# Performance work log

Measured on AMD Instinct MI355X. Metric: run time of the kernel, lower is better.

The kernel has to match this reference:

```python
import jax, jax.numpy as jnp
import numpy as np
import math

B, LT, LS, D, H, DFF = 4, 1024, 1024, 1024, 16, 4096
DK = D // H
EPS = 1e-5


def setup_inputs() -> dict:
    key = jax.random.key(0)
    ks = jax.random.split(key, 32)
    n = lambda i, shape, s=0.02: jax.random.normal(ks[i], shape, jnp.float32) * s
    inp = {
        'tgt': jax.random.normal(ks[0], (B, LT, D), jnp.float32),
        'memory': jax.random.normal(ks[1], (B, LS, D), jnp.float32),
        'src_pad_mask': jnp.zeros((B, LT, LS), dtype=bool),
        'tgt_mask': jnp.broadcast_to(jnp.triu(jnp.ones((LT, LT), dtype=bool), 1), (B, LT, LT)),
        # self-attention projections
        'self_wq': n(2, (D, D)), 'self_bq': jnp.zeros((D,)),
        'self_wk': n(3, (D, D)), 'self_bk': jnp.zeros((D,)),
        'self_wv': n(4, (D, D)), 'self_bv': jnp.zeros((D,)),
        'self_wo': n(5, (D, D)), 'self_bo': jnp.zeros((D,)),
        # cross-attention projections
        'cross_wq': n(6, (D, D)), 'cross_bq': jnp.zeros((D,)),
        'cross_wk': n(7, (D, D)), 'cross_bk': jnp.zeros((D,)),
        'cross_wv': n(8, (D, D)), 'cross_bv': jnp.zeros((D,)),
        'cross_wo': n(9, (D, D)), 'cross_bo': jnp.zeros((D,)),
        # layer norms (pre-norm)
        'ln1_g': jnp.ones((D,)), 'ln1_b': jnp.zeros((D,)),
        'ln2_g': jnp.ones((D,)), 'ln2_b': jnp.zeros((D,)),
        'ln3_g': jnp.ones((D,)), 'ln3_b': jnp.zeros((D,)),
        # feed forward
        'ffn_w1': n(10, (D, DFF)), 'ffn_b1': jnp.zeros((DFF,)),
        'ffn_w2': n(11, (DFF, D)), 'ffn_b2': jnp.zeros((D,)),
    }
    return inp


def _layernorm(x, g, b):
    mu = jnp.mean(x, axis=-1, keepdims=True)
    var = jnp.mean(jnp.square(x - mu), axis=-1, keepdims=True)
    return (x - mu) * jax.lax.rsqrt(var + EPS) * g + b


def _mha(xq, xkv, wq, bq, wk, bk, wv, bv, wo, bo, mask):
    b, lq, d = xq.shape
    lk = xkv.shape[1]
    q = (xq @ wq + bq).reshape(b, lq, H, DK).transpose(0, 2, 1, 3) / math.sqrt(DK)
    k = (xkv @ wk + bk).reshape(b, lk, H, DK).transpose(0, 2, 1, 3)
    v = (xkv @ wv + bv).reshape(b, lk, H, DK).transpose(0, 2, 1, 3)
    scores = jnp.einsum('bhqd,bhkd->bhqk', q, k)  # [B,H,Lq,Lk]
    scores = jnp.where(mask[:, None], -1e18, scores)
    attn = jax.nn.softmax(scores, axis=-1)  # dropout p=0 (eval)
    ctx = jnp.einsum('bhqk,bhkd->bhqd', attn, v)
    ctx = ctx.transpose(0, 2, 1, 3).reshape(b, lq, d)
    return ctx @ wo + bo


def reference(tgt, memory, src_pad_mask, tgt_mask,
              self_wq, self_bq, self_wk, self_bk, self_wv, self_bv, self_wo, self_bo,
              cross_wq, cross_bq, cross_wk, cross_bk, cross_wv, cross_bv, cross_wo, cross_bo,
              ln1_g, ln1_b, ln2_g, ln2_b, ln3_g, ln3_b,
              ffn_w1, ffn_b1, ffn_w2, ffn_b2):
    # pre-norm sublayer 1: self attention
    x = tgt + _mha(_layernorm(tgt, ln1_g, ln1_b), _layernorm(tgt, ln1_g, ln1_b),
                   self_wq, self_bq, self_wk, self_bk, self_wv, self_bv, self_wo, self_bo, tgt_mask)
    # pre-norm sublayer 2: cross attention
    x = x + _mha(_layernorm(x, ln2_g, ln2_b), memory,
                 cross_wq, cross_bq, cross_wk, cross_bk, cross_wv, cross_bv, cross_wo, cross_bo, src_pad_mask)
    # pre-norm sublayer 3: FFN
    h = _layernorm(x, ln3_g, ln3_b)
    x = x + (jax.nn.gelu(h @ ffn_w1 + ffn_b1) @ ffn_w2 + ffn_b2)
    return x
```

## Files before the change

kernel.cpp:

```cpp
#include <hip/hip_runtime.h>

typedef unsigned short u16;
typedef __attribute__((ext_vector_type(8))) __bf16 bf16x8;
typedef __attribute__((ext_vector_type(4))) float floatx4;

__device__ inline float bf2f(u16 u) {
    union { unsigned int i; float f; } x; x.i = ((unsigned int)u) << 16; return x.f;
}
__device__ inline u16 f2bf(float f) {
    __bf16 h = (__bf16)f; return __builtin_bit_cast(unsigned short, h);
}
__device__ inline float load_f(u16 v) { return bf2f(v); }
__device__ inline float load_f(float v) { return v; }

__device__ inline floatx4 mfma_bf16(bf16x8 a, bf16x8 b, floatx4 c) {
    return __builtin_amdgcn_mfma_f32_16x16x32_bf16(a, b, c, 0, 0, 0);
}

__device__ inline float gelu_tanh(float x) {
    float u = 0.7978845608028654f * (x + 0.044715f * x * x * x);
    u = fminf(fmaxf(u, -15.f), 15.f);
    float e = __expf(2.f * u);
    float th = (e - 1.f) / (e + 1.f);
    return 0.5f * x * (1.f + th);
}

__device__ inline void async16(const void* g, void* l) {
    __builtin_amdgcn_global_load_lds(
        (const __attribute__((address_space(1))) unsigned int*)g,
        (__attribute__((address_space(3))) unsigned int*)l, 16, 0, 0);
}

__global__ __launch_bounds__(256)
void detect_dtype(const u16* __restrict__ p, int* __restrict__ flag) {
    int t = threadIdx.x, cnt = 0;
    #pragma unroll
    for (int j = 0; j < 8; ++j) {
        unsigned e = (p[t * 8 + j] >> 7) & 0xFF;
        cnt += (e >= 100 && e <= 140) ? 1 : 0;
    }
    __shared__ int s[256];
    s[t] = cnt; __syncthreads();
    for (int off = 128; off; off >>= 1) { if (t < off) s[t] += s[t + off]; __syncthreads(); }
    if (t == 0) *flag = (s[0] < 1844) ? 1 : 0;
}

__global__ __launch_bounds__(256)
void convert_big(const void* __restrict__ tgt, const void* __restrict__ mem,
                 u16* __restrict__ tgt_c, u16* __restrict__ mem_c,
                 float* __restrict__ X, const int* __restrict__ flag) {
    int f = *flag;
    int b = blockIdx.x;
    bool isT = b < 4096;
    const void* s = isT ? tgt : mem;
    u16* d = isT ? tgt_c : mem_c;
    int i = (((isT ? b : b - 4096) * 256) + threadIdx.x) * 4;
    #pragma unroll
    for (int j = 0; j < 4; ++j) {
        float v; u16 hv;
        if (f) { v = ((const float*)s)[i + j]; hv = f2bf(v); }
        else   { hv = ((const u16*)s)[i + j]; v = bf2f(hv); }
        d[i + j] = hv;
        if (isT) X[i + j] = v;
    }
}

struct VecTab { const void* src[16]; int n[16]; int off[16]; };
__global__ __launch_bounds__(256)
void convert_vecs(VecTab tab, u16* __restrict__ dst, const int* __restrict__ flag) {
    int f = *flag;
    int b = blockIdx.x;
    const void* s = tab.src[b];
    int n = tab.n[b];
    u16* d = dst + tab.off[b];
    for (int i = threadIdx.x; i < n; i += 256)
        d[i] = f ? f2bf(((const float*)s)[i]) : ((const u16*)s)[i];
}

__global__ __launch_bounds__(256)
void store_out(const float* __restrict__ X, void* __restrict__ out, int n,
               const int* __restrict__ flag) {
    int f = *flag;
    int i = (blockIdx.x * 256 + threadIdx.x) * 4;
    if (i < n) {
        #pragma unroll
        for (int j = 0; j < 4; ++j) {
            float v = X[i + j];
            if (f) ((float*)out)[i + j] = v;
            else   ((u16*)out)[i + j] = f2bf(v);
        }
    }
}

struct TransTab {
    const void* src[10]; u16* dst[10];
    int C[10]; int start[10];
};
__global__ __launch_bounds__(256)
void transpose_batch(TransTab tb, const int* __restrict__ flag) {
    int f = *flag;
    int bid = blockIdx.x;
    int seg = 0;
    #pragma unroll
    for (int i = 1; i < 10; ++i) if (bid >= tb.start[i]) seg = i;
    int local = bid - tb.start[seg];
    const void* src = tb.src[seg];
    u16* dst = tb.dst[seg];
    int C = tb.C[seg];
    int ct = C >> 5;
    int by = local / ct, bx = local - by * ct;
    int R = (seg < 8) ? 1024 : ((seg == 8) ? 1024 : 4096);
    __shared__ u16 tile[32][33];
    int tx = threadIdx.x & 31, ty = threadIdx.x >> 5;
    int r0 = by * 32, c0 = bx * 32;
    #pragma unroll
    for (int i = 0; i < 32; i += 8) {
        size_t idx = (size_t)(r0 + ty + i) * C + c0 + tx;
        tile[ty + i][tx] = f ? f2bf(((const float*)src)[idx]) : ((const u16*)src)[idx];
    }
    __syncthreads();
    #pragma unroll
    for (int i = 0; i < 32; i += 8)
        dst[(size_t)(c0 + ty + i) * R + r0 + tx] = tile[tx][ty + i];
}

template <typename TIN>
__global__ __launch_bounds__(256)
void lnorm(const TIN* __restrict__ Xin, const u16* __restrict__ gg,
           const u16* __restrict__ bb, u16* __restrict__ Y) {
    const int row = blockIdx.x, t = threadIdx.x;
    const TIN* xr = Xin + (size_t)row * 1024;
    float x[4]; float s1 = 0.f, s2 = 0.f;
    #pragma unroll
    for (int i = 0; i < 4; ++i) {
        float v = load_f(xr[i * 256 + t]);
        x[i] = v; s1 += v; s2 += v * v;
    }
    #pragma unroll
    for (int m = 1; m < 64; m <<= 1) { s1 += __shfl_xor(s1, m, 64); s2 += __shfl_xor(s2, m, 64); }
    __shared__ float red[8];
    if ((t & 63) == 0) { red[(t >> 6) * 2] = s1; red[(t >> 6) * 2 + 1] = s2; }
    __syncthreads();
    s1 = red[0] + red[2] + red[4] + red[6];
    s2 = red[1] + red[3] + red[5] + red[7];
    float mu = s1 * (1.f / 1024.f);
    float var = s2 * (1.f / 1024.f) - mu * mu;
    float rs = rsqrtf(var + 1e-5f);
    #pragma unroll
    for (int i = 0; i < 4; ++i) {
        int idx = i * 256 + t;
        float yv = (x[i] - mu) * rs * bf2f(gg[idx]) + bf2f(bb[idx]);
        Y[(size_t)row * 1024 + idx] = f2bf(yv);
    }
}

template <int TM>
__global__ __launch_bounds__(256, 4)
void gemm_bt2(const u16* __restrict__ A, const u16* __restrict__ Bt,
              const u16* __restrict__ bias, u16* __restrict__ C,
              float* __restrict__ Xres, int M, int N, int K, int ldc, int epi) {
    __shared__ alignas(16) u16 As[TM * 32];
    __shared__ alignas(16) u16 Bs[128 * 32];
    constexpr int MI = TM / 32;
    constexpr int AROWS = TM / 4;
    const int t = threadIdx.x;
    const int lane = t & 63, w = t >> 6;
    const int l15 = lane & 15, quad = lane >> 4;
    const int m0 = blockIdx.y * TM, n0 = blockIdx.x * 128;
    const int wm = (w >> 1) * (TM / 2), wn = (w & 1) * 64;
    const int ksl = K / gridDim.z;
    const int kb = blockIdx.z * ksl, ke = kb + ksl;
    const int srow = lane >> 2, scol = (lane & 3) * 8;
    const u16* ga = A + (size_t)(m0 + w * AROWS + srow) * K + scol;
    const u16* gb = Bt + (size_t)(n0 + w * 32 + srow) * K + scol;
    u16* lA = &As[(w * AROWS) * 32];
    u16* lB0 = &Bs[(w * 32) * 32];
    u16* lB1 = &Bs[(w * 32 + 16) * 32];
    floatx4 acc[MI][4] = {};

    for (int k0 = kb; k0 < ke; k0 += 32) {
        __syncthreads();
        #pragma unroll
        for (int c = 0; c < TM / 64; ++c)
            async16(ga + (size_t)(c * 16) * K + k0, lA + c * 16 * 32);
        async16(gb + k0, lB0);
        async16(gb + (size_t)16 * K + k0, lB1);
        __syncthreads();
        bf16x8 af[MI], bfr[4];
        #pragma unroll
        for (int i = 0; i < MI; ++i)
            af[i] = *(const bf16x8*)&As[(wm + i * 16 + l15) * 32 + quad * 8];
        #pragma unroll
        for (int i = 0; i < 4; ++i)
            bfr[i] = *(const bf16x8*)&Bs[(wn + i * 16 + l15) * 32 + quad * 8];
        #pragma unroll
        for (int mi = 0; mi < MI; ++mi)
            #pragma unroll
            for (int ni = 0; ni < 4; ++ni)
                acc[mi][ni] = mfma_bf16(af[mi], bfr[ni], acc[mi][ni]);
    }

    const bool addb = (blockIdx.z == 0);
    #pragma unroll
    for (int mi = 0; mi < MI; ++mi) {
        #pragma unroll
        for (int ni = 0; ni < 4; ++ni) {
            int gn = n0 + wn + ni * 16 + l15;
            float bv = addb ? bf2f(bias[gn]) : 0.f;
            #pragma unroll
            for (int r = 0; r < 4; ++r) {
                int gm = m0 + wm + mi * 16 + quad * 4 + r;
                float v = acc[mi][ni][r] + bv;
                size_t idx = (size_t)gm * ldc + gn;
                if (epi == 0)      C[idx] = f2bf(v);
                else if (epi == 1) C[idx] = f2bf(gelu_tanh(v));
                else if (epi == 2) Xres[idx] += v;
                else               atomicAdd(&Xres[idx], v);
            }
        }
    }
}

#define SCL2 0.18033688011112042f
__global__ __launch_bounds__(256, 4)
void attn_fwd2(const u16* __restrict__ QKV, u16* __restrict__ CTX, int causal) {
    __shared__ alignas(16) u16 Ks[64 * 72];
    __shared__ alignas(16) u16 Vst[64 * 72];
    __shared__ alignas(16) u16 Sw[4][16 * 72];
    const int t = threadIdx.x;
    const int lane = t & 63, w = t >> 6;
    const int l15 = lane & 15, quad = lane >> 4;
    const int q0 = blockIdx.x * 64, h = blockIdx.y, b = blockIdx.z;
    const int qrow = q0 + w * 16 + l15;
    const u16* qp = QKV + (size_t)(b * 1024 + qrow) * 3072 + h * 64;
    bf16x8 aq0 = *(const bf16x8*)(qp + quad * 8);
    bf16x8 aq1 = *(const bf16x8*)(qp + 32 + quad * 8);
    floatx4 O[4] = {};
    float mo[4], lo[4];
    #pragma unroll
    for (int r = 0; r < 4; ++r) { mo[r] = -1e30f; lo[r] = 0.f; }

    const int skey = t >> 2, snn = t & 3, sd0 = (t & 3) * 16;
    const int swz = skey ^ (snn << 3);
    const int kend = causal ? (q0 + 64) : 1024;
    for (int kt = 0; kt < kend; kt += 64) {
        __syncthreads();
        {
            const u16* kvb = QKV + (size_t)(b * 1024 + kt + skey) * 3072 + h * 64 + sd0;
            bf16x8 k0v = *(const bf16x8*)(kvb + 1024);
            bf16x8 k1v = *(const bf16x8*)(kvb + 1024 + 8);
            *(bf16x8*)&Ks[skey * 72 + sd0] = k0v;
            *(bf16x8*)&Ks[skey * 72 + sd0 + 8] = k1v;
            bf16x8 v0v = *(const bf16x8*)(kvb + 2048);
            bf16x8 v1v = *(const bf16x8*)(kvb + 2048 + 8);
            #pragma unroll
            for (int j = 0; j < 8; ++j) Vst[(sd0 + j) * 72 + swz] = ((u16*)&v0v)[j];
            #pragma unroll
            for (int j = 0; j < 8; ++j) Vst[(sd0 + 8 + j) * 72 + swz] = ((u16*)&v1v)[j];
        }
        __syncthreads();
        floatx4 S[4];
        #pragma unroll
        for (int kg = 0; kg < 4; ++kg) {
            bf16x8 bk0 = *(const bf16x8*)&Ks[(kg * 16 + l15) * 72 + quad * 8];
            bf16x8 bk1 = *(const bf16x8*)&Ks[(kg * 16 + l15) * 72 + 32 + quad * 8];
            floatx4 z = {};
            z = mfma_bf16(aq0, bk0, z);
            z = mfma_bf16(aq1, bk1, z);
            S[kg] = z;
        }
        const bool domask = causal && (kt == q0);
        float al[4];
        #pragma unroll
        for (int r = 0; r < 4; ++r) {
            #pragma unroll
            for (int kg = 0; kg < 4; ++kg) {
                float s = S[kg][r] * SCL2;
                if (domask) {
                    int kg_glob = kt + kg * 16 + l15;
                    int qg = q0 + w * 16 + quad * 4 + r;
                    if (kg_glob > qg) s = -1e30f;
                }
                S[kg][r] = s;
            }
            float v = fmaxf(fmaxf(S[0][r], S[1][r]), fmaxf(S[2][r], S[3][r]));
            #pragma unroll
            for (int msk = 1; msk < 16; msk <<= 1) v = fmaxf(v, __shfl_xor(v, msk, 64));
            float mn = fmaxf(mo[r], v);
            al[r] = exp2f(mo[r] - mn);
            float ssum = 0.f;
            #pragma unroll
            for (int kg = 0; kg < 4; ++kg) {
                float p = exp2f(S[kg][r] - mn);
                S[kg][r] = p; ssum += p;
            }
            #pragma unroll
            for (int msk = 1; msk < 16; msk <<= 1) ssum += __shfl_xor(ssum, msk, 64);
            lo[r] = lo[r] * al[r] + ssum;
            mo[r] = mn;
        }
        #pragma unroll
        for (int kg = 0; kg < 4; ++kg)
            #pragma unroll
            for (int r = 0; r < 4; ++r)
                Sw[w][(quad * 4 + r) * 72 + kg * 16 + l15] = f2bf(S[kg][r]);
        #pragma unroll
        for (int g = 0; g < 4; ++g)
            #pragma unroll
            for (int r = 0; r < 4; ++r)
                O[g][r] *= al[r];
        bf16x8 ap0 = *(const bf16x8*)&Sw[w][l15 * 72 + quad * 8];
        bf16x8 ap1 = *(const bf16x8*)&Sw[w][l15 * 72 + 32 + quad * 8];
        #pragma unroll
        for (int g = 0; g < 4; ++g) {
            bf16x8 bv0 = *(const bf16x8*)&Vst[(g * 16 + l15) * 72 + ((quad ^ g) << 3)];
            bf16x8 bv1 = *(const bf16x8*)&Vst[(g * 16 + l15) * 72 + 32 + ((quad ^ g) << 3)];
            O[g] = mfma_bf16(ap0, bv0, O[g]);
            O[g] = mfma_bf16(ap1, bv1, O[g]);
        }
    }
    #pragma unroll
    for (int r = 0; r < 4; ++r) {
        float inv = 1.0f / lo[r];
        int qg = q0 + w * 16 + quad * 4 + r;
        #pragma unroll
        for (int g = 0; g < 4; ++g)
            CTX[(size_t)(b * 1024 + qg) * 1024 + h * 64 + g * 16 + l15] = f2bf(O[g][r] * inv);
    }
}

extern "C" void kernel_launch(void* const* d_in, const int* in_sizes, int n_in,
                              void* d_out, int out_size, void* d_ws, size_t ws_size,
                              hipStream_t stream) {
    const void* tgt_raw    = d_in[0];
    const void* memory_raw = d_in[1];

    char* ws = (char*)d_ws;
    const size_t MiB = 1024 * 1024;
    float* X   = (float*)ws;
    u16* Y     = (u16*)(ws + 16 * MiB);
    u16* QKV   = (u16*)(ws + 24 * MiB);
    u16* CTX   = (u16*)(ws + 48 * MiB);
    u16* H1    = (u16*)(ws + 24 * MiB);
    u16* wt    = (u16*)(ws + 56 * MiB);
    u16* wqkv_s = wt;
    u16* wo_s  = wt + 3 * 1048576;
    u16* wq_c  = wt + 4 * 1048576;
    u16* wkv_c = wt + 5 * 1048576;
    u16* wo_c  = wt + 7 * 1048576;
    u16* w1t   = wt + 8 * 1048576;
    u16* w2t   = wt + 12 * 1048576;
    u16* tgt_c = (u16*)(ws + 88 * MiB);
    u16* mem_c = (u16*)(ws + 96 * MiB);
    u16* vecs  = (u16*)(ws + 104 * MiB);
    int* flag  = (int*)(ws + 105 * MiB);

    dim3 blk(256);
    detect_dtype<<<1, blk, 0, stream>>>((const u16*)tgt_raw, flag);
    convert_big<<<8192, blk, 0, stream>>>(tgt_raw, memory_raw, tgt_c, mem_c, X, flag);

    VecTab tab;
    const int srcIdx[16] = {5, 7, 9, 11, 13, 15, 17, 19, 20, 21, 22, 23, 24, 25, 27, 29};
    const int offs[16]   = {0, 1024, 2048, 3072, 4096, 5120, 6144, 7168,
                            8192, 9216, 10240, 11264, 12288, 13312, 14336, 18432};
    for (int i = 0; i < 16; ++i) {
        tab.src[i] = d_in[srcIdx[i]];
        tab.n[i] = (i == 14) ? 4096 : 1024;
        tab.off[i] = offs[i];
    }
    convert_vecs<<<16, blk, 0, stream>>>(tab, vecs, flag);
    u16* b_qkv_s = vecs;            u16* b_o_s  = vecs + 3072;
    u16* b_q_c   = vecs + 4096;     u16* b_kv_c = vecs + 5120;
    u16* b_o_c   = vecs + 7168;
    u16* g1 = vecs + 8192;  u16* be1 = vecs + 9216;
    u16* g2 = vecs + 10240; u16* be2 = vecs + 11264;
    u16* g3 = vecs + 12288; u16* be3 = vecs + 13312;
    u16* b_ff1 = vecs + 14336; u16* b_ff2 = vecs + 18432;

    TransTab tt;
    const void* tsrc[10] = {d_in[4], d_in[6], d_in[8], d_in[10], d_in[12],
                            d_in[14], d_in[16], d_in[18], d_in[26], d_in[28]};
    u16* tdst[10] = {wqkv_s, wqkv_s + 1048576, wqkv_s + 2 * 1048576, wo_s, wq_c,
                     wkv_c, wkv_c + 1048576, wo_c, w1t, w2t};
    int start = 0;
    for (int i = 0; i < 10; ++i) {
        tt.src[i] = tsrc[i]; tt.dst[i] = tdst[i];
        tt.C[i] = (i == 8) ? 4096 : 1024;
        tt.start[i] = start;
        int R = (i == 9) ? 4096 : 1024;
        start += (R / 32) * (tt.C[i] / 32);
    }
    transpose_batch<<<start, blk, 0, stream>>>(tt, flag);

    const int NTOK = 4096;
    dim3 gQKV(24, 32), gKV(16, 32), gFF1(32, 32);
    dim3 gN1k(8, 64);
    dim3 gFF2(8, 64, 2);
    dim3 ga(16, 16, 4);

    lnorm<u16><<<4096, blk, 0, stream>>>(tgt_c, g1, be1, Y);
    gemm_bt2<128><<<gQKV, blk, 0, stream>>>(Y, wqkv_s, b_qkv_s, QKV, nullptr, NTOK, 3072, 1024, 3072, 0);
    attn_fwd2<<<ga, blk, 0, stream>>>(QKV, CTX, 1);
    gemm_bt2<64><<<gN1k, blk, 0, stream>>>(CTX, wo_s, b_o_s, nullptr, X, NTOK, 1024, 1024, 1024, 2);

    lnorm<float><<<4096, blk, 0, stream>>>(X, g2, be2, Y);
    gemm_bt2<64><<<gN1k, blk, 0, stream>>>(Y, wq_c, b_q_c, QKV, nullptr, NTOK, 1024, 1024, 3072, 0);
    gemm_bt2<128><<<gKV, blk, 0, stream>>>(mem_c, wkv_c, b_kv_c, QKV + 1024, nullptr, NTOK, 2048, 1024, 3072, 0);
    attn_fwd2<<<ga, blk, 0, stream>>>(QKV, CTX, 0);
    gemm_bt2<64><<<gN1k, blk, 0, stream>>>(CTX, wo_c, b_o_c, nullptr, X, NTOK, 1024, 1024, 1024, 2);

    lnorm<float><<<4096, blk, 0, stream>>>(X, g3, be3, Y);
    gemm_bt2<128><<<gFF1, blk, 0, stream>>>(Y, w1t, b_ff1, H1, nullptr, NTOK, 4096, 1024, 4096, 1);
    gemm_bt2<64><<<gFF2, blk, 0, stream>>>(H1, w2t, b_ff2, nullptr, X, NTOK, 1024, 4096, 1024, 3);

    store_out<<<4096, blk, 0, stream>>>(X, d_out, NTOK * 1024, flag);
}
```

Measured before the change: 672.3 us.

## Deepen GEMM K-tile to 64 with XOR swizzle; 128-query attention blocks

```diff
diff --git a/kernel.cpp b/kernel.cpp
--- a/kernel.cpp
+++ b/kernel.cpp
@@ -156,13 +156,12 @@
 
 template <int TM>
 __global__ __launch_bounds__(256, 4)
-void gemm_bt2(const u16* __restrict__ A, const u16* __restrict__ Bt,
+void gemm_bt3(const u16* __restrict__ A, const u16* __restrict__ Bt,
               const u16* __restrict__ bias, u16* __restrict__ C,
               float* __restrict__ Xres, int M, int N, int K, int ldc, int epi) {
-    __shared__ alignas(16) u16 As[TM * 32];
-    __shared__ alignas(16) u16 Bs[128 * 32];
+    __shared__ alignas(16) u16 As[TM * 64];
+    __shared__ alignas(16) u16 Bs[128 * 64];
     constexpr int MI = TM / 32;
-    constexpr int AROWS = TM / 4;
     const int t = threadIdx.x;
     const int lane = t & 63, w = t >> 6;
     const int l15 = lane & 15, quad = lane >> 4;
@@ -170,34 +169,40 @@
     const int wm = (w >> 1) * (TM / 2), wn = (w & 1) * 64;
     const int ksl = K / gridDim.z;
     const int kb = blockIdx.z * ksl, ke = kb + ksl;
-    const int srow = lane >> 2, scol = (lane & 3) * 8;
-    const u16* ga = A + (size_t)(m0 + w * AROWS + srow) * K + scol;
+    const int srow = lane >> 3;
+    const int scol = ((lane & 7) ^ srow) * 8;
+    const u16* ga = A + (size_t)(m0 + w * (TM / 4) + srow) * K + scol;
     const u16* gb = Bt + (size_t)(n0 + w * 32 + srow) * K + scol;
-    u16* lA = &As[(w * AROWS) * 32];
-    u16* lB0 = &Bs[(w * 32) * 32];
-    u16* lB1 = &Bs[(w * 32 + 16) * 32];
+    u16* lA = &As[w * (TM / 4) * 64];
+    u16* lB = &Bs[w * 32 * 64];
     floatx4 acc[MI][4] = {};
-
-    for (int k0 = kb; k0 < ke; k0 += 32) {
+    const int rsw = l15 & 7;
+
+    for (int k0 = kb; k0 < ke; k0 += 64) {
         __syncthreads();
         #pragma unroll
-        for (int c = 0; c < TM / 64; ++c)
-            async16(ga + (size_t)(c * 16) * K + k0, lA + c * 16 * 32);
-        async16(gb + k0, lB0);
-        async16(gb + (size_t)16 * K + k0, lB1);
+        for (int c = 0; c < TM / 32; ++c)
+            async16(ga + (size_t)(c * 8) * K + k0, lA + c * 8 * 64);
+        #pragma unroll
+        for (int c = 0; c < 4; ++c)
+            async16(gb + (size_t)(c * 8) * K + k0, lB + c * 8 * 64);
         __syncthreads();
-        bf16x8 af[MI], bfr[4];
-        #pragma unroll
-        for (int i = 0; i < MI; ++i)
-            af[i] = *(const bf16x8*)&As[(wm + i * 16 + l15) * 32 + quad * 8];
-        #pragma unroll
-        for (int i = 0; i < 4; ++i)
-            bfr[i] = *(const bf16x8*)&Bs[(wn + i * 16 + l15) * 32 + quad * 8];
-        #pragma unroll
-        for (int mi = 0; mi < MI; ++mi)
-            #pragma unroll
-            for (int ni = 0; ni < 4; ++ni)
-                acc[mi][ni] = mfma_bf16(af[mi], bfr[ni], acc[mi][ni]);
+        #pragma unroll
+        for (int kh = 0; kh < 2; ++kh) {
+            const int cofs = ((kh * 4 + quad) ^ rsw) * 8;
+            bf16x8 af[MI], bfr[4];
+            #pragma unroll
+            for (int i = 0; i < MI; ++i)
+                af[i] = *(const bf16x8*)&As[(wm + i * 16 + l15) * 64 + cofs];
+            #pragma unroll
+            for (int i = 0; i < 4; ++i)
+                bfr[i] = *(const bf16x8*)&Bs[(wn + i * 16 + l15) * 64 + cofs];
+            #pragma unroll
+            for (int mi = 0; mi < MI; ++mi)
+                #pragma unroll
+                for (int ni = 0; ni < 4; ++ni)
+                    acc[mi][ni] = mfma_bf16(af[mi], bfr[ni], acc[mi][ni]);
+        }
     }
 
     const bool addb = (blockIdx.z == 0);
@@ -223,26 +228,31 @@
 
 #define SCL2 0.18033688011112042f
 __global__ __launch_bounds__(256, 4)
-void attn_fwd2(const u16* __restrict__ QKV, u16* __restrict__ CTX, int causal) {
+void attn_fwd3(const u16* __restrict__ QKV, u16* __restrict__ CTX, int causal) {
     __shared__ alignas(16) u16 Ks[64 * 72];
     __shared__ alignas(16) u16 Vst[64 * 72];
-    __shared__ alignas(16) u16 Sw[4][16 * 72];
+    __shared__ alignas(16) u16 Sw[4][32 * 72];
     const int t = threadIdx.x;
     const int lane = t & 63, w = t >> 6;
     const int l15 = lane & 15, quad = lane >> 4;
-    const int q0 = blockIdx.x * 64, h = blockIdx.y, b = blockIdx.z;
-    const int qrow = q0 + w * 16 + l15;
-    const u16* qp = QKV + (size_t)(b * 1024 + qrow) * 3072 + h * 64;
-    bf16x8 aq0 = *(const bf16x8*)(qp + quad * 8);
-    bf16x8 aq1 = *(const bf16x8*)(qp + 32 + quad * 8);
-    floatx4 O[4] = {};
-    float mo[4], lo[4];
-    #pragma unroll
-    for (int r = 0; r < 4; ++r) { mo[r] = -1e30f; lo[r] = 0.f; }
-
-    const int skey = t >> 2, snn = t & 3, sd0 = (t & 3) * 16;
-    const int swz = skey ^ (snn << 3);
-    const int kend = causal ? (q0 + 64) : 1024;
+    const int q0 = blockIdx.x * 128, h = blockIdx.y, b = blockIdx.z;
+    bf16x8 aq[2][2];
+    #pragma unroll
+    for (int g = 0; g < 2; ++g) {
+        const u16* qp = QKV + (size_t)(b * 1024 + q0 + w * 32 + g * 16 + l15) * 3072 + h * 64;
+        aq[g][0] = *(const bf16x8*)(qp + quad * 8);
+        aq[g][1] = *(const bf16x8*)(qp + 32 + quad * 8);
+    }
+    floatx4 O[2][4] = {};
+    float mo[2][4], lo[2][4];
+    #pragma unroll
+    for (int g = 0; g < 2; ++g)
+        #pragma unroll
+        for (int r = 0; r < 4; ++r) { mo[g][r] = -1e30f; lo[g][r] = 0.f; }
+
+    const int skey = t >> 2, sd0 = (t & 3) * 16;
+    const int swz = skey ^ ((t & 3) << 3);
+    const int kend = causal ? (q0 + 128) : 1024;
     for (int kt = 0; kt < kend; kt += 64) {
         __syncthreads();
         {
@@ -259,74 +269,89 @@
             for (int j = 0; j < 8; ++j) Vst[(sd0 + 8 + j) * 72 + swz] = ((u16*)&v1v)[j];
         }
         __syncthreads();
-        floatx4 S[4];
-        #pragma unroll
-        for (int kg = 0; kg < 4; ++kg) {
-            bf16x8 bk0 = *(const bf16x8*)&Ks[(kg * 16 + l15) * 72 + quad * 8];
-            bf16x8 bk1 = *(const bf16x8*)&Ks[(kg * 16 + l15) * 72 + 32 + quad * 8];
-            floatx4 z = {};
-            z = mfma_bf16(aq0, bk0, z);
-            z = mfma_bf16(aq1, bk1, z);
-            S[kg] = z;
-        }
-        const bool domask = causal && (kt == q0);
-        float al[4];
+        const bool domask = causal && (kt + 64 > q0);
+        float al[2][4];
+        #pragma unroll
+        for (int g = 0; g < 2; ++g) {
+            floatx4 S[4];
+            #pragma unroll
+            for (int kg = 0; kg < 4; ++kg) {
+                bf16x8 bk0 = *(const bf16x8*)&Ks[(kg * 16 + l15) * 72 + quad * 8];
+                bf16x8 bk1 = *(const bf16x8*)&Ks[(kg * 16 + l15) * 72 + 32 + quad * 8];
+                floatx4 z = {};
+                z = mfma_bf16(aq[g][0], bk0, z);
+                z = mfma_bf16(aq[g][1], bk1, z);
+                S[kg] = z;
+            }
+            #pragma unroll
+            for (int r = 0; r < 4; ++r) {
+                #pragma unroll
+                for (int kg = 0; kg < 4; ++kg) {
+                    float s = S[kg][r] * SCL2;
+                    if (domask) {
+                        int kg_glob = kt + kg * 16 + l15;
+                        int qg = q0 + w * 32 + g * 16 + quad * 4 + r;
+                        if (kg_glob > qg) s = -1e30f;
+                    }
+                    S[kg][r] = s;
+                }
+                float v = fmaxf(fmaxf(S[0][r], S[1][r]), fmaxf(S[2][r], S[3][r]));
+                #pragma unroll
+                for (int msk = 1; msk < 16; msk <<= 1) v = fmaxf(v, __shfl_xor(v, msk, 64));
+                float mn = fmaxf(mo[g][r], v);
+                al[g][r] = exp2f(mo[g][r] - mn);
+                float ssum = 0.f;
+                #pragma unroll
+                for (int kg = 0; kg < 4; ++kg) {
+                    float p = exp2f(S[kg][r] - mn);
+                    S[kg][r] = p; ssum += p;
+                }
+                #pragma unroll
+                for (int msk = 1; msk < 16; msk <<= 1) ssum += __shfl_xor(ssum, msk, 64);
+                lo[g][r] = lo[g][r] * al[g][r] + ssum;
+                mo[g][r] = mn;
+            }
+            #pragma unroll
+            for (int kg = 0; kg < 4; ++kg)
+                #pragma unroll
+                for (int r = 0; r < 4; ++r)
+                    Sw[w][(g * 16 + quad * 4 + r) * 72 + kg * 16 + l15] = f2bf(S[kg][r]);
+        }
+        #pragma unroll
+        for (int g = 0; g < 2; ++g)
+            #pragma unroll
+            for (int vg = 0; vg < 4; ++vg)
+                #pragma unroll
+                for (int r = 0; r < 4; ++r)
+                    O[g][vg][r] *= al[g][r];
+        bf16x8 ap[2][2];
+        #pragma unroll
+        for (int g = 0; g < 2; ++g) {
+            ap[g][0] = *(const bf16x8*)&Sw[w][(g * 16 + l15) * 72 + quad * 8];
+            ap[g][1] = *(const bf16x8*)&Sw[w][(g * 16 + l15) * 72 + 32 + quad * 8];
+        }
+        #pragma unroll
+        for (int vg = 0; vg < 4; ++vg) {
+            bf16x8 bv0 = *(const bf16x8*)&Vst[(vg * 16 + l15) * 72 + ((quad ^ vg) << 3)];
+            bf16x8 bv1 = *(const bf16x8*)&Vst[(vg * 16 + l15) * 72 + 32 + ((quad ^ vg) << 3)];
+            #pragma unroll
+            for (int g = 0; g < 2; ++g) {
+                O[g][vg] = mfma_bf16(ap[g][0], bv0, O[g][vg]);
+                O[g][vg] = mfma_bf16(ap[g][1], bv1, O[g][vg]);
+            }
+        }
+    }
+    #pragma unroll
+    for (int g = 0; g < 2; ++g)
         #pragma unroll
         for (int r = 0; r < 4; ++r) {
-            #pragma unroll
-            for (int kg = 0; kg < 4; ++kg) {
-                float s = S[kg][r] * SCL2;
-                if (domask) {
-                    int kg_glob = kt + kg * 16 + l15;
-                    int qg = q0 + w * 16 + quad * 4 + r;
-                    if (kg_glob > qg) s = -1e30f;
-                }
-                S[kg][r] = s;
-            }
-            float v = fmaxf(fmaxf(S[0][r], S[1][r]), fmaxf(S[2][r], S[3][r]));
-            #pragma unroll
-            for (int msk = 1; msk < 16; msk <<= 1) v = fmaxf(v, __shfl_xor(v, msk, 64));
-            float mn = fmaxf(mo[r], v);
-            al[r] = exp2f(mo[r] - mn);
-            float ssum = 0.f;
-            #pragma unroll
-            for (int kg = 0; kg < 4; ++kg) {
-                float p = exp2f(S[kg][r] - mn);
-                S[kg][r] = p; ssum += p;
-            }
-            #pragma unroll
-            for (int msk = 1; msk < 16; msk <<= 1) ssum += __shfl_xor(ssum, msk, 64);
-            lo[r] = lo[r] * al[r] + ssum;
-            mo[r] = mn;
-        }
-        #pragma unroll
-        for (int kg = 0; kg < 4; ++kg)
-            #pragma unroll
-            for (int r = 0; r < 4; ++r)
-                Sw[w][(quad * 4 + r) * 72 + kg * 16 + l15] = f2bf(S[kg][r]);
-        #pragma unroll
-        for (int g = 0; g < 4; ++g)
-            #pragma unroll
-            for (int r = 0; r < 4; ++r)
-                O[g][r] *= al[r];
-        bf16x8 ap0 = *(const bf16x8*)&Sw[w][l15 * 72 + quad * 8];
-        bf16x8 ap1 = *(const bf16x8*)&Sw[w][l15 * 72 + 32 + quad * 8];
-        #pragma unroll
-        for (int g = 0; g < 4; ++g) {
-            bf16x8 bv0 = *(const bf16x8*)&Vst[(g * 16 + l15) * 72 + ((quad ^ g) << 3)];
-            bf16x8 bv1 = *(const bf16x8*)&Vst[(g * 16 + l15) * 72 + 32 + ((quad ^ g) << 3)];
-            O[g] = mfma_bf16(ap0, bv0, O[g]);
-            O[g] = mfma_bf16(ap1, bv1, O[g]);
-        }
-    }
-    #pragma unroll
-    for (int r = 0; r < 4; ++r) {
-        float inv = 1.0f / lo[r];
-        int qg = q0 + w * 16 + quad * 4 + r;
-        #pragma unroll
-        for (int g = 0; g < 4; ++g)
-            CTX[(size_t)(b * 1024 + qg) * 1024 + h * 64 + g * 16 + l15] = f2bf(O[g][r] * inv);
-    }
+            float inv = 1.0f / lo[g][r];
+            int qg = q0 + w * 32 + g * 16 + quad * 4 + r;
+            #pragma unroll
+            for (int vg = 0; vg < 4; ++vg)
+                CTX[(size_t)(b * 1024 + qg) * 1024 + h * 64 + vg * 16 + l15] =
+                    f2bf(O[g][vg][r] * inv);
+        }
 }
 
 extern "C" void kernel_launch(void* const* d_in, const int* in_sizes, int n_in,
@@ -393,25 +418,27 @@
     transpose_batch<<<start, blk, 0, stream>>>(tt, flag);
 
     const int NTOK = 4096;
-    dim3 gQKV(24, 32), gKV(16, 32), gFF1(32, 32);
+    dim3 gQKV(24, 32);
+    dim3 gKV(16, 64);
+    dim3 gFF1(32, 32);
     dim3 gN1k(8, 64);
     dim3 gFF2(8, 64, 2);
-    dim3 ga(16, 16, 4);
+    dim3 ga(8, 16, 4);
 
     lnorm<u16><<<4096, blk, 0, stream>>>(tgt_c, g1, be1, Y);
-    gemm_bt2<128><<<gQKV, blk, 0, stream>>>(Y, wqkv_s, b_qkv_s, QKV, nullptr, NTOK, 3072, 1024, 3072, 0);
-    attn_fwd2<<<ga, blk, 0, stream>>>(QKV, CTX, 1);
-    gemm_bt2<64><<<gN1k, blk, 0, stream>>>(CTX, wo_s, b_o_s, nullptr, X, NTOK, 1024, 1024, 1024, 2);
+    gemm_bt3<128><<<gQKV, blk, 0, stream>>>(Y, wqkv_s, b_qkv_s, QKV, nullptr, NTOK, 3072, 1024, 3072, 0);
+    attn_fwd3<<<ga, blk, 0, stream>>>(QKV, CTX, 1);
+    gemm_bt3<64><<<gN1k, blk, 0, stream>>>(CTX, wo_s, b_o_s, nullptr, X, NTOK, 1024, 1024, 1024, 2);
 
     lnorm<float><<<4096, blk, 0, stream>>>(X, g2, be2, Y);
-    gemm_bt2<64><<<gN1k, blk, 0, stream>>>(Y, wq_c, b_q_c, QKV, nullptr, NTOK, 1024, 1024, 3072, 0);
-    gemm_bt2<128><<<gKV, blk, 0, stream>>>(mem_c, wkv_c, b_kv_c, QKV + 1024, nullptr, NTOK, 2048, 1024, 3072, 0);
-    attn_fwd2<<<ga, blk, 0, stream>>>(QKV, CTX, 0);
-    gemm_bt2<64><<<gN1k, blk, 0, stream>>>(CTX, wo_c, b_o_c, nullptr, X, NTOK, 1024, 1024, 1024, 2);
+    gemm_bt3<64><<<gN1k, blk, 0, stream>>>(Y, wq_c, b_q_c, QKV, nullptr, NTOK, 1024, 1024, 3072, 0);
+    gemm_bt3<64><<<gKV, blk, 0, stream>>>(mem_c, wkv_c, b_kv_c, QKV + 1024, nullptr, NTOK, 2048, 1024, 3072, 0);
+    attn_fwd3<<<ga, blk, 0, stream>>>(QKV, CTX, 0);
+    gemm_bt3<64><<<gN1k, blk, 0, stream>>>(CTX, wo_c, b_o_c, nullptr, X, NTOK, 1024, 1024, 1024, 2);
 
     lnorm<float><<<4096, blk, 0, stream>>>(X, g3, be3, Y);
-    gemm_bt2<128><<<gFF1, blk, 0, stream>>>(Y, w1t, b_ff1, H1, nullptr, NTOK, 4096, 1024, 4096, 1);
-    gemm_bt2<64><<<gFF2, blk, 0, stream>>>(H1, w2t, b_ff2, nullptr, X, NTOK, 1024, 4096, 1024, 3);
+    gemm_bt3<128><<<gFF1, blk, 0, stream>>>(Y, w1t, b_ff1, H1, nullptr, NTOK, 4096, 1024, 4096, 1);
+    gemm_bt3<64><<<gFF2, blk, 0, stream>>>(H1, w2t, b_ff2, nullptr, X, NTOK, 1024, 4096, 1024, 3);
 
     store_out<<<4096, blk, 0, stream>>>(X, d_out, NTOK * 1024, flag);
 }
```

Result: slower. 686.1 us (+2.1%).

## Widen GEMM K-tile to 64 with XOR-swizzled LDS and MFMA row-sum in attention

Applied to the files above, without the earlier changes.

```diff
diff --git a/kernel.cpp b/kernel.cpp
--- a/kernel.cpp
+++ b/kernel.cpp
@@ -156,13 +156,12 @@
 
 template <int TM>
 __global__ __launch_bounds__(256, 4)
-void gemm_bt2(const u16* __restrict__ A, const u16* __restrict__ Bt,
+void gemm_bt3(const u16* __restrict__ A, const u16* __restrict__ Bt,
               const u16* __restrict__ bias, u16* __restrict__ C,
               float* __restrict__ Xres, int M, int N, int K, int ldc, int epi) {
-    __shared__ alignas(16) u16 As[TM * 32];
-    __shared__ alignas(16) u16 Bs[128 * 32];
+    __shared__ alignas(16) u16 As[TM * 64];
+    __shared__ alignas(16) u16 Bs[128 * 64];
     constexpr int MI = TM / 32;
-    constexpr int AROWS = TM / 4;
     const int t = threadIdx.x;
     const int lane = t & 63, w = t >> 6;
     const int l15 = lane & 15, quad = lane >> 4;
@@ -170,34 +169,40 @@
     const int wm = (w >> 1) * (TM / 2), wn = (w & 1) * 64;
     const int ksl = K / gridDim.z;
     const int kb = blockIdx.z * ksl, ke = kb + ksl;
-    const int srow = lane >> 2, scol = (lane & 3) * 8;
-    const u16* ga = A + (size_t)(m0 + w * AROWS + srow) * K + scol;
+    const int srow = lane >> 3;
+    const int scol = ((lane & 7) ^ srow) * 8;
+    const u16* ga = A + (size_t)(m0 + w * (TM / 4) + srow) * K + scol;
     const u16* gb = Bt + (size_t)(n0 + w * 32 + srow) * K + scol;
-    u16* lA = &As[(w * AROWS) * 32];
-    u16* lB0 = &Bs[(w * 32) * 32];
-    u16* lB1 = &Bs[(w * 32 + 16) * 32];
+    u16* lA = &As[w * (TM / 4) * 64];
+    u16* lB = &Bs[w * 32 * 64];
     floatx4 acc[MI][4] = {};
-
-    for (int k0 = kb; k0 < ke; k0 += 32) {
+    const int rsw = l15 & 7;
+
+    for (int k0 = kb; k0 < ke; k0 += 64) {
         __syncthreads();
         #pragma unroll
-        for (int c = 0; c < TM / 64; ++c)
-            async16(ga + (size_t)(c * 16) * K + k0, lA + c * 16 * 32);
-        async16(gb + k0, lB0);
-        async16(gb + (size_t)16 * K + k0, lB1);
+        for (int c = 0; c < TM / 32; ++c)
+            async16(ga + (size_t)(c * 8) * K + k0, lA + c * 8 * 64);
+        #pragma unroll
+        for (int c = 0; c < 4; ++c)
+            async16(gb + (size_t)(c * 8) * K + k0, lB + c * 8 * 64);
         __syncthreads();
-        bf16x8 af[MI], bfr[4];
-        #pragma unroll
-        for (int i = 0; i < MI; ++i)
-            af[i] = *(const bf16x8*)&As[(wm + i * 16 + l15) * 32 + quad * 8];
-        #pragma unroll
-        for (int i = 0; i < 4; ++i)
-            bfr[i] = *(const bf16x8*)&Bs[(wn + i * 16 + l15) * 32 + quad * 8];
-        #pragma unroll
-        for (int mi = 0; mi < MI; ++mi)
-            #pragma unroll
-            for (int ni = 0; ni < 4; ++ni)
-                acc[mi][ni] = mfma_bf16(af[mi], bfr[ni], acc[mi][ni]);
+        #pragma unroll
+        for (int kh = 0; kh < 2; ++kh) {
+            const int cofs = ((kh * 4 + quad) ^ rsw) * 8;
+            bf16x8 af[MI], bfr[4];
+            #pragma unroll
+            for (int i = 0; i < MI; ++i)
+                af[i] = *(const bf16x8*)&As[(wm + i * 16 + l15) * 64 + cofs];
+            #pragma unroll
+            for (int i = 0; i < 4; ++i)
+                bfr[i] = *(const bf16x8*)&Bs[(wn + i * 16 + l15) * 64 + cofs];
+            #pragma unroll
+            for (int mi = 0; mi < MI; ++mi)
+                #pragma unroll
+                for (int ni = 0; ni < 4; ++ni)
+                    acc[mi][ni] = mfma_bf16(af[mi], bfr[ni], acc[mi][ni]);
+        }
     }
 
     const bool addb = (blockIdx.z == 0);
@@ -223,7 +228,7 @@
 
 #define SCL2 0.18033688011112042f
 __global__ __launch_bounds__(256, 4)
-void attn_fwd2(const u16* __restrict__ QKV, u16* __restrict__ CTX, int causal) {
+void attn_fwd4(const u16* __restrict__ QKV, u16* __restrict__ CTX, int causal) {
     __shared__ alignas(16) u16 Ks[64 * 72];
     __shared__ alignas(16) u16 Vst[64 * 72];
     __shared__ alignas(16) u16 Sw[4][16 * 72];
@@ -236,9 +241,13 @@
     bf16x8 aq0 = *(const bf16x8*)(qp + quad * 8);
     bf16x8 aq1 = *(const bf16x8*)(qp + 32 + quad * 8);
     floatx4 O[4] = {};
-    float mo[4], lo[4];
-    #pragma unroll
-    for (int r = 0; r < 4; ++r) { mo[r] = -1e30f; lo[r] = 0.f; }
+    floatx4 Os = {};
+    float mo[4];
+    #pragma unroll
+    for (int r = 0; r < 4; ++r) mo[r] = -1e30f;
+    bf16x8 ones;
+    #pragma unroll
+    for (int j = 0; j < 8; ++j) ones[j] = (__bf16)1.0f;
 
     const int skey = t >> 2, snn = t & 3, sd0 = (t & 3) * 16;
     const int swz = skey ^ (snn << 3);
@@ -288,15 +297,9 @@
             for (int msk = 1; msk < 16; msk <<= 1) v = fmaxf(v, __shfl_xor(v, msk, 64));
             float mn = fmaxf(mo[r], v);
             al[r] = exp2f(mo[r] - mn);
-            float ssum = 0.f;
-            #pragma unroll
-            for (int kg = 0; kg < 4; ++kg) {
-                float p = exp2f(S[kg][r] - mn);
-                S[kg][r] = p; ssum += p;
-            }
-            #pragma unroll
-            for (int msk = 1; msk < 16; msk <<= 1) ssum += __shfl_xor(ssum, msk, 64);
-            lo[r] = lo[r] * al[r] + ssum;
+            #pragma unroll
+            for (int kg = 0; kg < 4; ++kg)
+                S[kg][r] = exp2f(S[kg][r] - mn);
             mo[r] = mn;
         }
         #pragma unroll
@@ -309,6 +312,8 @@
             #pragma unroll
             for (int r = 0; r < 4; ++r)
                 O[g][r] *= al[r];
+        #pragma unroll
+        for (int r = 0; r < 4; ++r) Os[r] *= al[r];
         bf16x8 ap0 = *(const bf16x8*)&Sw[w][l15 * 72 + quad * 8];
         bf16x8 ap1 = *(const bf16x8*)&Sw[w][l15 * 72 + 32 + quad * 8];
         #pragma unroll
@@ -318,10 +323,12 @@
             O[g] = mfma_bf16(ap0, bv0, O[g]);
             O[g] = mfma_bf16(ap1, bv1, O[g]);
         }
+        Os = mfma_bf16(ap0, ones, Os);
+        Os = mfma_bf16(ap1, ones, Os);
     }
     #pragma unroll
     for (int r = 0; r < 4; ++r) {
-        float inv = 1.0f / lo[r];
+        float inv = 1.0f / Os[r];
         int qg = q0 + w * 16 + quad * 4 + r;
         #pragma unroll
         for (int g = 0; g < 4; ++g)
@@ -393,25 +400,27 @@
     transpose_batch<<<start, blk, 0, stream>>>(tt, flag);
 
     const int NTOK = 4096;
-    dim3 gQKV(24, 32), gKV(16, 32), gFF1(32, 32);
+    dim3 gQKV(24, 32);
+    dim3 gKV(16, 64);
+    dim3 gFF1(32, 32);
     dim3 gN1k(8, 64);
     dim3 gFF2(8, 64, 2);
     dim3 ga(16, 16, 4);
 
     lnorm<u16><<<4096, blk, 0, stream>>>(tgt_c, g1, be1, Y);
-    gemm_bt2<128><<<gQKV, blk, 0, stream>>>(Y, wqkv_s, b_qkv_s, QKV, nullptr, NTOK, 3072, 1024, 3072, 0);
-    attn_fwd2<<<ga, blk, 0, stream>>>(QKV, CTX, 1);
-    gemm_bt2<64><<<gN1k, blk, 0, stream>>>(CTX, wo_s, b_o_s, nullptr, X, NTOK, 1024, 1024, 1024, 2);
+    gemm_bt3<128><<<gQKV, blk, 0, stream>>>(Y, wqkv_s, b_qkv_s, QKV, nullptr, NTOK, 3072, 1024, 3072, 0);
+    attn_fwd4<<<ga, blk, 0, stream>>>(QKV, CTX, 1);
+    gemm_bt3<64><<<gN1k, blk, 0, stream>>>(CTX, wo_s, b_o_s, nullptr, X, NTOK, 1024, 1024, 1024, 2);
 
     lnorm<float><<<4096, blk, 0, stream>>>(X, g2, be2, Y);
-    gemm_bt2<64><<<gN1k, blk, 0, stream>>>(Y, wq_c, b_q_c, QKV, nullptr, NTOK, 1024, 1024, 3072, 0);
-    gemm_bt2<128><<<gKV, blk, 0, stream>>>(mem_c, wkv_c, b_kv_c, QKV + 1024, nullptr, NTOK, 2048, 1024, 3072, 0);
-    attn_fwd2<<<ga, blk, 0, stream>>>(QKV, CTX, 0);
-    gemm_bt2<64><<<gN1k, blk, 0, stream>>>(CTX, wo_c, b_o_c, nullptr, X, NTOK, 1024, 1024, 1024, 2);
+    gemm_bt3<64><<<gN1k, blk, 0, stream>>>(Y, wq_c, b_q_c, QKV, nullptr, NTOK, 1024, 1024, 3072, 0);
+    gemm_bt3<64><<<gKV, blk, 0, stream>>>(mem_c, wkv_c, b_kv_c, QKV + 1024, nullptr, NTOK, 2048, 1024, 3072, 0);
+    attn_fwd4<<<ga, blk, 0, stream>>>(QKV, CTX, 0);
+    gemm_bt3<64><<<gN1k, blk, 0, stream>>>(CTX, wo_c, b_o_c, nullptr, X, NTOK, 1024, 1024, 1024, 2);
 
     lnorm<float><<<4096, blk, 0, stream>>>(X, g3, be3, Y);
-    gemm_bt2<128><<<gFF1, blk, 0, stream>>>(Y, w1t, b_ff1, H1, nullptr, NTOK, 4096, 1024, 4096, 1);
-    gemm_bt2<64><<<gFF2, blk, 0, stream>>>(H1, w2t, b_ff2, nullptr, X, NTOK, 1024, 4096, 1024, 3);
+    gemm_bt3<128><<<gFF1, blk, 0, stream>>>(Y, w1t, b_ff1, H1, nullptr, NTOK, 4096, 1024, 4096, 1);
+    gemm_bt3<64><<<gFF2, blk, 0, stream>>>(H1, w2t, b_ff2, nullptr, X, NTOK, 1024, 4096, 1024, 3);
 
     store_out<<<4096, blk, 0, stream>>>(X, d_out, NTOK * 1024, flag);
 }
```

Measured after the change: 642.2 us. -4.5%, faster.
